# Kernel tuning notes

Measured on AMD Instinct MI355X. Metric: run time of the kernel, lower is better.

The kernel has to match this reference:

```python
import jax, jax.numpy as jnp
import numpy as np

N = 4096; B = 4; NPB = N // B; K = 16
C = 128; COUT = 128; LMAX = 2; L = (LMAX + 1) ** 2  # 9 SH coefficients
H = 8; A = 8; V = 16; HV = H * V
F = 256; NB = 128; FD = 256; CUTOFF = 3.0
E = N * K

def _silu(x):
    return x * jax.nn.sigmoid(x)

def _mish(x):
    return x * jnp.tanh(jax.nn.softplus(x))

def _rms_norm(x, gamma):
    # degree-wise RMS over channel dim, x: [N, L, C]
    s = jnp.sqrt(jnp.mean(x * x, axis=-1, keepdims=True) + 1e-6)
    return x / s * gamma

def _rot_l1(x, R):
    # rotate the l=1 block (coeffs 1:4) of x [E, L, C] by R [E, 3, 3]
    l1 = jnp.einsum('eij,ejc->eic', R, x[:, 1:4, :])
    return jnp.concatenate([x[:, :1, :], l1, x[:, 4:, :]], axis=1)

def _knn(coord, batch):
    d2 = jnp.sum((coord[:, None, :] - coord[None, :, :]) ** 2, axis=-1)  # [N,N]
    same = batch[:, None] == batch[None, :]
    big = jnp.asarray(1e9, d2.dtype)
    d2 = jnp.where(same, d2, big)
    d2 = d2.at[jnp.arange(N), jnp.arange(N)].set(big)
    neg, idx = jax.lax.top_k(-d2, K)
    dist = jnp.sqrt(jnp.maximum(-neg, 0.0))
    edge_src = idx.reshape(-1)                       # [E]
    edge_dst = jnp.repeat(jnp.arange(N), K)          # [E]
    valid = (dist <= CUTOFF).reshape(-1)
    return edge_src, edge_dst, valid

def _edge_rot_mat(edge_vec):
    # deterministic rotation aligning each edge with the y-axis (eSCN-style)
    nx = edge_vec / (jnp.linalg.norm(edge_vec, axis=-1, keepdims=True) + 1e-12)
    ref = jnp.where(jnp.abs(nx[:, :1]) < 0.9,
                    jnp.array([1.0, 0.0, 0.0], nx.dtype),
                    jnp.array([0.0, 1.0, 0.0], nx.dtype))
    nz = jnp.cross(nx, ref)
    nz = nz / (jnp.linalg.norm(nz, axis=-1, keepdims=True) + 1e-12)
    ny = jnp.cross(nz, nx)
    return jnp.stack([nz, nx, ny], axis=1)  # [E,3,3]; R @ edge_dir = e_y

def _forward(node_coord, node_emb, batch, condition,
             W_e1, b_e1, W_e2, b_e2, W_src, W_dst, w_a, W_v, W_o,
             gamma1, gamma2, W_g, W_f1, W_f2, W_film, b_film):
    # dynamic KNN graph; geometry detached as in original (edge_vec.detach())
    coord_g = jax.lax.stop_gradient(node_coord)
    edge_src, edge_dst, valid = _knn(coord_g, batch)
    edge_vec = coord_g[edge_src] - coord_g[edge_dst]                  # [E,3]
    edge_len = jnp.linalg.norm(edge_vec, axis=-1)                     # [E]
    R = _edge_rot_mat(edge_vec)                                       # [E,3,3]
    # gaussian radial basis -> per-edge embedding
    mu = jnp.linspace(0.0, CUTOFF, NB)
    sigma = CUTOFF / NB
    rbf = jnp.exp(-0.5 * ((edge_len[:, None] - mu) / sigma) ** 2)     # [E,NB]
    edge_h = _silu(rbf @ W_e1 + b_e1) @ W_e2 + b_e2                   # [E,HV]
    # equivariant attention (rotate into edge frame, attend, rotate back)
    x_src = _rot_l1(node_emb[edge_src], R)                            # [E,L,C]
    q = node_emb[edge_dst, 0] @ W_dst + x_src[:, 0] @ W_src           # [E,H*A]
    logits = jnp.einsum('eha,ha->eh', _silu(q).reshape(E, H, A), w_a)
    logits = jnp.where(valid[:, None], logits, -1e9)
    m = jax.ops.segment_max(logits, edge_dst, num_segments=N)
    ex = jnp.exp(logits - m[edge_dst])
    den = jax.ops.segment_sum(ex, edge_dst, num_segments=N)
    attn = ex / (den[edge_dst] + 1e-9)                                # [E,H]
    v = jnp.einsum('elc,cv->elv', x_src, W_v) * edge_h[:, None, :]    # [E,L,HV]
    v = v.reshape(E, L, H, V) * attn[:, None, :, None]
    msg = _rot_l1(v.reshape(E, L, HV), jnp.swapaxes(R, 1, 2))         # back to global frame
    agg = jax.ops.segment_sum(msg, edge_dst, num_segments=N)          # [N,L,HV]
    x = node_emb + jnp.einsum('nlv,vc->nlc', agg, W_o)
    # FFN with separable S2 (scalar-gated) activation
    h = _rms_norm(x, gamma2)
    gate = _silu(h[:, 0] @ W_g)                                       # [N,F]
    hid = jnp.einsum('nlc,cf->nlf', h, W_f1) * gate[:, None, :]
    x = x + jnp.einsum('nlf,fo->nlo', hid, W_f2)
    x = _rms_norm(x, gamma1)
    # FiLM conditioning over flattened (L*C) per batch element
    film = _mish(condition) @ W_film + b_film                         # [B, 2*L*COUT]
    w, bfi = film[:, :L * COUT], film[:, L * COUT:]
    c = x.reshape(B, NPB, L * COUT) * w[:, None, :] + bfi[:, None, :]
    return c.reshape(N, L, COUT)

def setup_inputs():
    key = jax.random.key(0)
    ks = jax.random.split(key, 16)
    node_coord = jax.random.uniform(ks[0], (N, 3)) * 2.0
    node_emb = jax.random.normal(ks[1], (N, L, C)) * 0.1
    batch = jnp.arange(N, dtype=jnp.int64 if jax.config.jax_enable_x64 else jnp.int32) // NPB
    condition = jax.random.normal(ks[2], (B, FD))
    s = lambda d: 1.0 / np.sqrt(d)
    return {
        'node_coord': node_coord, 'node_emb': node_emb, 'batch': batch, 'condition': condition,
        'W_e1': jax.random.normal(ks[3], (NB, 128)) * s(NB), 'b_e1': jnp.zeros((128,)),
        'W_e2': jax.random.normal(ks[4], (128, HV)) * s(128), 'b_e2': jnp.zeros((HV,)),
        'W_src': jax.random.normal(ks[5], (C, H * A)) * s(C),
        'W_dst': jax.random.normal(ks[6], (C, H * A)) * s(C),
        'w_a': jax.random.normal(ks[7], (H, A)) * s(A),
        'W_v': jax.random.normal(ks[8], (C, HV)) * s(C),
        'W_o': jax.random.normal(ks[9], (HV, C)) * s(HV),
        'gamma1': jnp.ones((C,)), 'gamma2': jnp.ones((C,)),
        'W_g': jax.random.normal(ks[10], (C, F)) * s(C),
        'W_f1': jax.random.normal(ks[11], (C, F)) * s(C),
        'W_f2': jax.random.normal(ks[12], (F, COUT)) * s(F),
        'W_film': jax.random.normal(ks[13], (FD, 2 * L * COUT)) * s(FD),
        'b_film': jnp.zeros((2 * L * COUT,)),
    }

def reference(node_coord, node_emb, batch, condition,
              W_e1, b_e1, W_e2, b_e2, W_src, W_dst, w_a, W_v, W_o,
              gamma1, gamma2, W_g, W_f1, W_f2, W_film, b_film):
    out = _forward(node_coord, node_emb, batch, condition,
                   W_e1, b_e1, W_e2, b_e2, W_src, W_dst, w_a, W_v, W_o,
                   gamma1, gamma2, W_g, W_f1, W_f2, W_film, b_film)
    return (node_coord, out, batch)
```

## Files before the change

### kernel.cpp

```cpp
#include <hip/hip_runtime.h>

#define NNODE 4096
#define NPB   1024

typedef float v2f __attribute__((ext_vector_type(2)));
typedef float v4f __attribute__((ext_vector_type(4)));

__device__ __forceinline__ float siluf(float x){ return x / (1.0f + expf(-x)); }

__device__ __forceinline__ v2f pk_fma_lo(v2f a, v2f b, v2f c){
  v2f d;
  asm("v_pk_fma_f32 %0, %1, %2, %3 op_sel_hi:[1,0,1]" : "=v"(d) : "v"(a), "v"(b), "v"(c));
  return d;
}
__device__ __forceinline__ v2f pk_fma_hi(v2f a, v2f b, v2f c){
  v2f d;
  asm("v_pk_fma_f32 %0, %1, %2, %3 op_sel:[0,1,0] op_sel_hi:[1,1,1]" : "=v"(d) : "v"(a), "v"(b), "v"(c));
  return d;
}
__device__ __forceinline__ v2f pk_fma2(v2f a, v2f b, v2f c){
  v2f d;
  asm("v_pk_fma_f32 %0, %1, %2, %3" : "=v"(d) : "v"(a), "v"(b), "v"(c));
  return d;
}
#define SHLO(h) __builtin_shufflevector((h), (h), 0, 1)
#define SHHI(h) __builtin_shufflevector((h), (h), 2, 3)

__global__ __launch_bounds__(256) void k_film(const float* __restrict__ cond,
                                              const float* __restrict__ Wfilm,
                                              const float* __restrict__ bfilm,
                                              float* __restrict__ filmG){
  __shared__ float mL[256];
  int b = blockIdx.y;
  int t = threadIdx.x;
  int j = blockIdx.x*256 + t;
  float x = cond[b*256 + t];
  float sp = fmaxf(x, 0.f) + log1pf(expf(-fabsf(x)));
  mL[t] = x * tanhf(sp);
  __syncthreads();
  if(j >= 2304) return;
  float acc = bfilm[j];
  for(int i=0;i<256;i++) acc += mL[i] * Wfilm[i*2304 + j];
  filmG[b*2304 + j] = acc;
}

__global__ __launch_bounds__(256) void k_pre(const float* __restrict__ emb,
                                             const float* __restrict__ Wv,
                                             const float* __restrict__ Wsrc,
                                             const float* __restrict__ Wdst,
                                             float* __restrict__ ZG,
                                             float* __restrict__ QsG,
                                             float* __restrict__ QdG){
  __shared__ __align__(16) float S[4*1152];
  const int t = threadIdx.x;
  const int rg = __builtin_amdgcn_readfirstlane(t >> 6);
  const int lane = t & 63;
  const int c0 = lane*2;
  const int n0 = blockIdx.x*4;
  const int n = n0 + rg;

  {
    const float4* src = (const float4*)(emb + (size_t)n0*1152);
    float4* dst = (float4*)S;
    for(int i=t; i<1152; i+=256) dst[i] = src[i];
  }
  __syncthreads();
  const float* en = &S[rg*1152];

  v2f z[9];
  #pragma unroll
  for(int l=0;l<9;l++) z[l] = (v2f)0.0f;
  for(int c4=0;c4<32;c4++){
    v2f wv0 = *(const v2f*)&Wv[(c4*4+0)*128 + c0];
    v2f wv1 = *(const v2f*)&Wv[(c4*4+1)*128 + c0];
    v2f wv2 = *(const v2f*)&Wv[(c4*4+2)*128 + c0];
    v2f wv3 = *(const v2f*)&Wv[(c4*4+3)*128 + c0];
    #pragma unroll
    for(int l=0;l<9;l++){
      v4f x4 = *(const v4f*)&en[l*128 + c4*4];
      v2f h01 = SHLO(x4), h23 = SHHI(x4);
      z[l] = pk_fma_lo(wv0, h01, z[l]);
      z[l] = pk_fma_hi(wv1, h01, z[l]);
      z[l] = pk_fma_lo(wv2, h23, z[l]);
      z[l] = pk_fma_hi(wv3, h23, z[l]);
    }
  }
  #pragma unroll
  for(int l=0;l<9;l++) *(v2f*)&ZG[(size_t)n*1152 + l*128 + c0] = z[l];

  float qs = 0.f, qd = 0.f;
  for(int c4=0;c4<32;c4++){
    v4f e4 = *(const v4f*)&en[c4*4];
    qs = fmaf(e4.x, Wsrc[(c4*4+0)*64 + lane], qs);
    qs = fmaf(e4.y, Wsrc[(c4*4+1)*64 + lane], qs);
    qs = fmaf(e4.z, Wsrc[(c4*4+2)*64 + lane], qs);
    qs = fmaf(e4.w, Wsrc[(c4*4+3)*64 + lane], qs);
    qd = fmaf(e4.x, Wdst[(c4*4+0)*64 + lane], qd);
    qd = fmaf(e4.y, Wdst[(c4*4+1)*64 + lane], qd);
    qd = fmaf(e4.z, Wdst[(c4*4+2)*64 + lane], qd);
    qd = fmaf(e4.w, Wdst[(c4*4+3)*64 + lane], qd);
  }
  QsG[n*64 + lane] = qs;
  QdG[n*64 + lane] = qd;
}

#define E2_HD   0
#define E2_RB   2048
#define E2_AT   2304
#define E2_KI   2432
#define E2_LEN  2448
#define E2_VL   2464
#define E2_W0   2480
#define F_ACT   0
#define F_HID   1152
#define E2_NPF  2560
__global__ __launch_bounds__(128, 4) void k_node(
    const float* __restrict__ coord,
    const float* __restrict__ emb,
    const float* __restrict__ We1, const float* __restrict__ be1,
    const float* __restrict__ We2, const float* __restrict__ be2,
    const float* __restrict__ wa,
    const float* __restrict__ Wo,
    const float* __restrict__ g1, const float* __restrict__ g2,
    const float* __restrict__ Wg, const float* __restrict__ Wf1,
    const float* __restrict__ Wf2,
    const float* __restrict__ Qs, const float* __restrict__ Qd,
    const float* __restrict__ Z,
    const float* __restrict__ filmG,
    float* __restrict__ out){
  __shared__ __align__(16) float S[2*E2_NPF];
  int* Si = (int*)S;
  const int t = threadIdx.x;
  const int w = __builtin_amdgcn_readfirstlane(t >> 6);
  const int lane = t & 63;
  const int bid = blockIdx.x;
  const int sbid = (bid & 7) * (NNODE/16) + (bid >> 3);
  const int n = sbid*2 + w;
  const int base = n & ~(NPB - 1);
  const int self = n - base;
  const int NP = w * E2_NPF;
  const int c0 = lane*2;
  const int myh = lane >> 3;

  {
    const float* cb = coord + (size_t)base*3;
    const float cx = cb[self*3+0];
    const float cy = cb[self*3+1];
    const float cz = cb[self*3+2];
    float d2a[16]; int ida[16];
    #pragma unroll
    for(int q=0;q<16;q++){
      int j = lane + q*64;
      float dx = __fsub_rn(cb[j*3+0], cx);
      float dy = __fsub_rn(cb[j*3+1], cy);
      float dz = __fsub_rn(cb[j*3+2], cz);
      float d2 = __fadd_rn(__fadd_rn(__fmul_rn(dx,dx), __fmul_rn(dy,dy)), __fmul_rn(dz,dz));
      if(j == self) d2 = 3e38f;
      d2a[q] = d2; ida[q] = j;
    }
    #pragma unroll 1
    for(int r=0;r<16;r++){
      float bd = d2a[0]; int bi = ida[0];
      #pragma unroll
      for(int q=1;q<16;q++){
        bool bet = (d2a[q] < bd) || (d2a[q] == bd && ida[q] < bi);
        if(bet){ bd = d2a[q]; bi = ida[q]; }
      }
      #pragma unroll
      for(int s=1;s<64;s<<=1){
        float od = __shfl_xor(bd, s, 64);
        int   oi = __shfl_xor(bi, s, 64);
        bool bet = (od < bd) || (od == bd && oi < bi);
        if(bet){ bd = od; bi = oi; }
      }
      if(lane == 0){
        Si[NP + E2_KI + r] = bi;
        float len = __fsqrt_rn(bd);
        S[NP + E2_LEN + r] = len;
        S[NP + E2_VL + r]  = (len <= 3.0f) ? 1.0f : 0.0f;
        int i0 = (int)(len * (127.0f/3.0f) + 0.5f);
        int w0 = i0 - 7;
        w0 = w0 < 0 ? 0 : (w0 > 112 ? 112 : w0);
        Si[NP + E2_W0 + r] = w0;
      }
      #pragma unroll
      for(int q=0;q<16;q++) if(ida[q] == bi) d2a[q] = 3e38f;
    }
  }
  __syncthreads();

  {
    const int e0 = lane >> 3, hh = lane & 7;
    float4 qda = *(const float4*)&Qd[(size_t)n*64 + hh*8];
    float4 qdb = *(const float4*)&Qd[(size_t)n*64 + hh*8 + 4];
    float4 waa = *(const float4*)&wa[hh*8];
    float4 wab = *(const float4*)&wa[hh*8 + 4];
    float lg[2];
    #pragma unroll
    for(int s=0;s<2;s++){
      int e = e0 + s*8;
      int src = base + Si[NP + E2_KI + e];
      float4 qa = *(const float4*)&Qs[(size_t)src*64 + hh*8];
      float4 qb = *(const float4*)&Qs[(size_t)src*64 + hh*8 + 4];
      float sv = siluf(qda.x+qa.x)*waa.x + siluf(qda.y+qa.y)*waa.y
               + siluf(qda.z+qa.z)*waa.z + siluf(qda.w+qa.w)*waa.w
               + siluf(qdb.x+qb.x)*wab.x + siluf(qdb.y+qb.y)*wab.y
               + siluf(qdb.z+qb.z)*wab.z + siluf(qdb.w+qb.w)*wab.w;
      lg[s] = (S[NP + E2_VL + e] > 0.5f) ? sv : -1e9f;
    }
    float m = fmaxf(lg[0], lg[1]);
    m = fmaxf(m, __shfl_xor(m, 8, 64));
    m = fmaxf(m, __shfl_xor(m, 16, 64));
    m = fmaxf(m, __shfl_xor(m, 32, 64));
    float ex0 = expf(lg[0] - m), ex1 = expf(lg[1] - m);
    float den = ex0 + ex1;
    den += __shfl_xor(den, 8, 64);
    den += __shfl_xor(den, 16, 64);
    den += __shfl_xor(den, 32, 64);
    float inv = 1.0f/(den + 1e-9f);
    S[NP + E2_AT + lane]      = ex0*inv;
    S[NP + E2_AT + 64 + lane] = ex1*inv;

    const float step = 3.0f/127.0f;
    const float sigma = 3.0f/128.0f;
    #pragma unroll
    for(int k=0;k<4;k++){
      int idx = lane + k*64;
      int e = idx >> 4, wi = idx & 15;
      float len = S[NP + E2_LEN + e];
      int bin = Si[NP + E2_W0 + e] + wi;
      float d = (len - step*(float)bin) / sigma;
      S[NP + E2_RB + idx] = expf(-0.5f*d*d);
    }
  }
  __syncthreads();

  {
    float a4[16][2]; int b0e[16];
    #pragma unroll
    for(int e=0;e<16;e++){ a4[e][0]=0.f; a4[e][1]=0.f; b0e[e] = Si[NP + E2_W0 + e]; }
    #pragma unroll 1
    for(int wi=0; wi<16; wi++){
      #pragma unroll
      for(int e=0;e<16;e++){
        float rb = S[NP + E2_RB + e*16 + wi];
        float2 we = *(const float2*)&We1[(size_t)(b0e[e] + wi)*128 + c0];
        a4[e][0] = fmaf(rb, we.x, a4[e][0]);
        a4[e][1] = fmaf(rb, we.y, a4[e][1]);
      }
    }
    float2 b1v = *(const float2*)&be1[c0];
    #pragma unroll
    for(int e=0;e<16;e++){
      float2 o; o.x = siluf(a4[e][0] + b1v.x); o.y = siluf(a4[e][1] + b1v.y);
      *(float2*)&S[NP + E2_HD + e*128 + c0] = o;
    }
  }
  __syncthreads();

  v2f a5[16];
  #pragma unroll
  for(int e=0;e<16;e++) a5[e] = (v2f)0.0f;
  #pragma unroll 1
  for(int c4=0;c4<32;c4++){
    v2f w0 = *(const v2f*)&We2[(c4*4+0)*128 + c0];
    v2f w1 = *(const v2f*)&We2[(c4*4+1)*128 + c0];
    v2f w2 = *(const v2f*)&We2[(c4*4+2)*128 + c0];
    v2f w3 = *(const v2f*)&We2[(c4*4+3)*128 + c0];
    #pragma unroll
    for(int e=0;e<16;e++){
      v4f h4 = *(const v4f*)&S[NP + E2_HD + e*128 + c4*4];
      v2f h01 = SHLO(h4), h23 = SHHI(h4);
      a5[e] = pk_fma_lo(w0, h01, a5[e]);
      a5[e] = pk_fma_hi(w1, h01, a5[e]);
      a5[e] = pk_fma_lo(w2, h23, a5[e]);
      a5[e] = pk_fma_hi(w3, h23, a5[e]);
    }
  }

  {
    v2f b2v = *(const v2f*)&be2[c0];
    v2f ag[9];
    #pragma unroll
    for(int l=0;l<9;l++) ag[l] = (v2f)0.0f;
    #pragma unroll 4
    for(int e=0;e<16;e++){
      int src = base + Si[NP + E2_KI + e];
      const float* zp = &Z[(size_t)src*1152 + c0];
      float at = S[NP + E2_AT + e*8 + myh];
      v2f sc = (a5[e] + b2v) * at;
      #pragma unroll
      for(int l=0;l<9;l++){
        v2f z2 = *(const v2f*)&zp[l*128];
        ag[l] = pk_fma2(z2, sc, ag[l]);
      }
    }
    #pragma unroll
    for(int l=0;l<9;l++) *(v2f*)&S[NP + F_ACT + l*128 + c0] = ag[l];
  }

  float* W_ = &S[NP];

  v2f x[9];
  #pragma unroll
  for(int l=0;l<9;l++) x[l] = (v2f)0.0f;
  #pragma unroll 1
  for(int c4=0;c4<32;c4++){
    v2f w0 = *(const v2f*)&Wo[(c4*4+0)*128 + c0];
    v2f w1 = *(const v2f*)&Wo[(c4*4+1)*128 + c0];
    v2f w2 = *(const v2f*)&Wo[(c4*4+2)*128 + c0];
    v2f w3 = *(const v2f*)&Wo[(c4*4+3)*128 + c0];
    #pragma unroll
    for(int l=0;l<9;l++){
      v4f a4 = *(const v4f*)&W_[F_ACT + l*128 + c4*4];
      v2f h01 = SHLO(a4), h23 = SHHI(a4);
      x[l] = pk_fma_lo(w0, h01, x[l]);
      x[l] = pk_fma_hi(w1, h01, x[l]);
      x[l] = pk_fma_lo(w2, h23, x[l]);
      x[l] = pk_fma_hi(w3, h23, x[l]);
    }
  }

  {
    float g2a = g2[c0], g2b = g2[c0+1];
    #pragma unroll
    for(int l=0;l<9;l++){
      v2f e2 = *(const v2f*)&emb[(size_t)n*1152 + l*128 + c0];
      x[l] += e2;
      float sq = x[l][0]*x[l][0] + x[l][1]*x[l][1];
      #pragma unroll
      for(int s=1;s<64;s<<=1) sq += __shfl_xor(sq, s, 64);
      float ss = sqrtf(sq/128.f + 1e-6f);
      v2f o; o.x = x[l][0]/ss*g2a; o.y = x[l][1]/ss*g2b;
      *(v2f*)&W_[F_ACT + l*128 + c0] = o;
    }
  }

  #pragma unroll 1
  for(int ft=0;ft<2;ft++){
    v2f ha[9]; v2f ga = (v2f)0.0f;
    #pragma unroll
    for(int l=0;l<9;l++) ha[l] = (v2f)0.0f;
    #pragma unroll 1
    for(int c4=0;c4<32;c4++){
      v2f wf0 = *(const v2f*)&Wf1[(c4*4+0)*256 + ft*128 + c0];
      v2f wf1 = *(const v2f*)&Wf1[(c4*4+1)*256 + ft*128 + c0];
      v2f wf2 = *(const v2f*)&Wf1[(c4*4+2)*256 + ft*128 + c0];
      v2f wf3 = *(const v2f*)&Wf1[(c4*4+3)*256 + ft*128 + c0];
      v2f wg0 = *(const v2f*)&Wg [(c4*4+0)*256 + ft*128 + c0];
      v2f wg1 = *(const v2f*)&Wg [(c4*4+1)*256 + ft*128 + c0];
      v2f wg2 = *(const v2f*)&Wg [(c4*4+2)*256 + ft*128 + c0];
      v2f wg3 = *(const v2f*)&Wg [(c4*4+3)*256 + ft*128 + c0];
      v4f h0 = *(const v4f*)&W_[F_ACT + 0*128 + c4*4];
      v2f h01 = SHLO(h0), h23 = SHHI(h0);
      ga = pk_fma_lo(wg0, h01, ga);
      ga = pk_fma_hi(wg1, h01, ga);
      ga = pk_fma_lo(wg2, h23, ga);
      ga = pk_fma_hi(wg3, h23, ga);
      ha[0] = pk_fma_lo(wf0, h01, ha[0]);
      ha[0] = pk_fma_hi(wf1, h01, ha[0]);
      ha[0] = pk_fma_lo(wf2, h23, ha[0]);
      ha[0] = pk_fma_hi(wf3, h23, ha[0]);
      #pragma unroll
      for(int l=1;l<9;l++){
        v4f h4 = *(const v4f*)&W_[F_ACT + l*128 + c4*4];
        v2f a01 = SHLO(h4), a23 = SHHI(h4);
        ha[l] = pk_fma_lo(wf0, a01, ha[l]);
        ha[l] = pk_fma_hi(wf1, a01, ha[l]);
        ha[l] = pk_fma_lo(wf2, a23, ha[l]);
        ha[l] = pk_fma_hi(wf3, a23, ha[l]);
      }
    }
    float gx = siluf(ga[0]), gy = siluf(ga[1]);
    #pragma unroll
    for(int l=0;l<9;l++){
      v2f o; o.x = ha[l][0]*gx; o.y = ha[l][1]*gy;
      *(v2f*)&W_[F_HID + l*128 + c0] = o;
    }
    #pragma unroll 1
    for(int f4=0;f4<32;f4++){
      v2f w0 = *(const v2f*)&Wf2[(ft*128 + f4*4+0)*128 + c0];
      v2f w1 = *(const v2f*)&Wf2[(ft*128 + f4*4+1)*128 + c0];
      v2f w2 = *(const v2f*)&Wf2[(ft*128 + f4*4+2)*128 + c0];
      v2f w3 = *(const v2f*)&Wf2[(ft*128 + f4*4+3)*128 + c0];
      #pragma unroll
      for(int l=0;l<9;l++){
        v4f h4 = *(const v4f*)&W_[F_HID + l*128 + f4*4];
        v2f h01 = SHLO(h4), h23 = SHHI(h4);
        x[l] = pk_fma_lo(w0, h01, x[l]);
        x[l] = pk_fma_hi(w1, h01, x[l]);
        x[l] = pk_fma_lo(w2, h23, x[l]);
        x[l] = pk_fma_hi(w3, h23, x[l]);
      }
    }
  }

  {
    float g1a = g1[c0], g1b = g1[c0+1];
    int b = n >> 10;
    #pragma unroll
    for(int l=0;l<9;l++){
      float sq = x[l][0]*x[l][0] + x[l][1]*x[l][1];
      #pragma unroll
      for(int s=1;s<64;s<<=1) sq += __shfl_xor(sq, s, 64);
      float ss = sqrtf(sq/128.f + 1e-6f);
      v2f fw = *(const v2f*)&filmG[b*2304 + l*128 + c0];
      v2f fb = *(const v2f*)&filmG[b*2304 + 1152 + l*128 + c0];
      v2f o;
      o.x = x[l][0]/ss*g1a*fw.x + fb.x;
      o.y = x[l][1]/ss*g1b*fw.y + fb.y;
      *(v2f*)&out[12288 + (size_t)n*1152 + l*128 + c0] = o;
    }
  }
}

__global__ __launch_bounds__(256) void k_copy(const float* __restrict__ coord,
                                              float* __restrict__ out){
  int i = blockIdx.x*256 + threadIdx.x;
  if(i < 12288) out[i] = coord[i];
  int n = i - 12288;
  if(n >= 0 && n < 4096) out[12288 + 4718592 + n] = (float)(n >> 10);
}

extern "C" void kernel_launch(void* const* d_in, const int* in_sizes, int n_in,
                              void* d_out, int out_size, void* d_ws, size_t ws_size,
                              hipStream_t stream) {
  const float* coord = (const float*)d_in[0];
  const float* emb   = (const float*)d_in[1];
  const float* cond  = (const float*)d_in[3];
  const float* We1   = (const float*)d_in[4];
  const float* be1   = (const float*)d_in[5];
  const float* We2   = (const float*)d_in[6];
  const float* be2   = (const float*)d_in[7];
  const float* Wsrc  = (const float*)d_in[8];
  const float* Wdst  = (const float*)d_in[9];
  const float* wa    = (const float*)d_in[10];
  const float* Wv    = (const float*)d_in[11];
  const float* Wo    = (const float*)d_in[12];
  const float* g1    = (const float*)d_in[13];
  const float* g2    = (const float*)d_in[14];
  const float* Wg    = (const float*)d_in[15];
  const float* Wf1   = (const float*)d_in[16];
  const float* Wf2   = (const float*)d_in[17];
  const float* Wfilm = (const float*)d_in[18];
  const float* bfilm = (const float*)d_in[19];

  float* outf  = (float*)d_out;
  float* filmG = (float*)d_ws;
  float* QsG   = filmG + 9216;
  float* QdG   = QsG + 262144;
  float* ZG    = QdG + 262144;

  k_film<<<dim3(9,4), 256, 0, stream>>>(cond, Wfilm, bfilm, filmG);
  k_pre<<<NNODE/4, 256, 0, stream>>>(emb, Wv, Wsrc, Wdst, ZG, QsG, QdG);
  k_node<<<NNODE/2, 128, 0, stream>>>(coord, emb,
                                      We1, be1, We2, be2, wa,
                                      Wo, g1, g2, Wg, Wf1, Wf2,
                                      QsG, QdG, ZG, filmG, outf);
  k_copy<<<64, 256, 0, stream>>>(coord, outf);
}
```

Measured before the change: 361.3 us.

## Broadcast node activations via readlane into SGPRs instead of LDS round-trips

Replaces the LDS staging of per-node activations (aggregated messages, normalized hidden, gated FFN hidden) with v_readlane broadcasts into scalar registers that feed packed FMAs directly. This removes LDS stores, LDS vector loads and the implied barriers in the three dense matmul chains. The cost is many readlane instructions (four per FMA group) on the scalar path, possible VALU-to-SGPR hazard stalls, and heavier register pressure from holding activations in VGPRs. Correctness depends on each wavefront holding a whole node's 128 channels, two per lane.

```diff
diff --git a/kernel.cpp b/kernel.cpp
--- a/kernel.cpp
+++ b/kernel.cpp
@@ -22,6 +22,14 @@
   v2f d;
   asm("v_pk_fma_f32 %0, %1, %2, %3" : "=v"(d) : "v"(a), "v"(b), "v"(c));
   return d;
+}
+__device__ __forceinline__ v2f pk_fma_sb(v2f a, unsigned long long b, v2f c){
+  v2f d;
+  asm("v_pk_fma_f32 %0, %1, %2, %3 op_sel_hi:[1,0,1]" : "=v"(d) : "v"(a), "s"(b), "v"(c));
+  return d;
+}
+__device__ __forceinline__ unsigned long long rlz(float v, int ln){
+  return (unsigned long long)(unsigned int)__builtin_amdgcn_readlane(__float_as_int(v), ln);
 }
 #define SHLO(h) __builtin_shufflevector((h), (h), 0, 1)
 #define SHHI(h) __builtin_shufflevector((h), (h), 2, 3)
@@ -111,8 +119,6 @@
 #define E2_LEN  2448
 #define E2_VL   2464
 #define E2_W0   2480
-#define F_ACT   0
-#define F_HID   1152
 #define E2_NPF  2560
 __global__ __launch_bounds__(128, 4) void k_node(
     const float* __restrict__ coord,
@@ -278,9 +284,9 @@
     }
   }
 
+  v2f ag[9];
   {
     v2f b2v = *(const v2f*)&be2[c0];
-    v2f ag[9];
     #pragma unroll
     for(int l=0;l<9;l++) ag[l] = (v2f)0.0f;
     #pragma unroll 4
@@ -295,32 +301,33 @@
         ag[l] = pk_fma2(z2, sc, ag[l]);
       }
     }
-    #pragma unroll
-    for(int l=0;l<9;l++) *(v2f*)&S[NP + F_ACT + l*128 + c0] = ag[l];
-  }
-
-  float* W_ = &S[NP];
+  }
+
 
   v2f x[9];
   #pragma unroll
   for(int l=0;l<9;l++) x[l] = (v2f)0.0f;
   #pragma unroll 1
   for(int c4=0;c4<32;c4++){
+    int ln0 = c4*2, ln1 = ln0+1;
     v2f w0 = *(const v2f*)&Wo[(c4*4+0)*128 + c0];
     v2f w1 = *(const v2f*)&Wo[(c4*4+1)*128 + c0];
     v2f w2 = *(const v2f*)&Wo[(c4*4+2)*128 + c0];
     v2f w3 = *(const v2f*)&Wo[(c4*4+3)*128 + c0];
     #pragma unroll
     for(int l=0;l<9;l++){
-      v4f a4 = *(const v4f*)&W_[F_ACT + l*128 + c4*4];
-      v2f h01 = SHLO(a4), h23 = SHHI(a4);
-      x[l] = pk_fma_lo(w0, h01, x[l]);
-      x[l] = pk_fma_hi(w1, h01, x[l]);
-      x[l] = pk_fma_lo(w2, h23, x[l]);
-      x[l] = pk_fma_hi(w3, h23, x[l]);
-    }
-  }
-
+      unsigned long long h0 = rlz(ag[l][0], ln0);
+      unsigned long long h1 = rlz(ag[l][1], ln0);
+      unsigned long long h2 = rlz(ag[l][0], ln1);
+      unsigned long long h3 = rlz(ag[l][1], ln1);
+      x[l] = pk_fma_sb(w0, h0, x[l]);
+      x[l] = pk_fma_sb(w1, h1, x[l]);
+      x[l] = pk_fma_sb(w2, h2, x[l]);
+      x[l] = pk_fma_sb(w3, h3, x[l]);
+    }
+  }
+
+  v2f hl[9];
   {
     float g2a = g2[c0], g2b = g2[c0+1];
     #pragma unroll
@@ -331,8 +338,8 @@
       #pragma unroll
       for(int s=1;s<64;s<<=1) sq += __shfl_xor(sq, s, 64);
       float ss = sqrtf(sq/128.f + 1e-6f);
-      v2f o; o.x = x[l][0]/ss*g2a; o.y = x[l][1]/ss*g2b;
-      *(v2f*)&W_[F_ACT + l*128 + c0] = o;
+      hl[l][0] = x[l][0]/ss*g2a;
+      hl[l][1] = x[l][1]/ss*g2b;
     }
   }
 
@@ -343,6 +350,7 @@
     for(int l=0;l<9;l++) ha[l] = (v2f)0.0f;
     #pragma unroll 1
     for(int c4=0;c4<32;c4++){
+      int ln0 = c4*2, ln1 = ln0+1;
       v2f wf0 = *(const v2f*)&Wf1[(c4*4+0)*256 + ft*128 + c0];
       v2f wf1 = *(const v2f*)&Wf1[(c4*4+1)*256 + ft*128 + c0];
       v2f wf2 = *(const v2f*)&Wf1[(c4*4+2)*256 + ft*128 + c0];
@@ -351,46 +359,52 @@
       v2f wg1 = *(const v2f*)&Wg [(c4*4+1)*256 + ft*128 + c0];
       v2f wg2 = *(const v2f*)&Wg [(c4*4+2)*256 + ft*128 + c0];
       v2f wg3 = *(const v2f*)&Wg [(c4*4+3)*256 + ft*128 + c0];
-      v4f h0 = *(const v4f*)&W_[F_ACT + 0*128 + c4*4];
-      v2f h01 = SHLO(h0), h23 = SHHI(h0);
-      ga = pk_fma_lo(wg0, h01, ga);
-      ga = pk_fma_hi(wg1, h01, ga);
-      ga = pk_fma_lo(wg2, h23, ga);
-      ga = pk_fma_hi(wg3, h23, ga);
-      ha[0] = pk_fma_lo(wf0, h01, ha[0]);
-      ha[0] = pk_fma_hi(wf1, h01, ha[0]);
-      ha[0] = pk_fma_lo(wf2, h23, ha[0]);
-      ha[0] = pk_fma_hi(wf3, h23, ha[0]);
+      {
+        unsigned long long h0 = rlz(hl[0][0], ln0);
+        unsigned long long h1 = rlz(hl[0][1], ln0);
+        unsigned long long h2 = rlz(hl[0][0], ln1);
+        unsigned long long h3 = rlz(hl[0][1], ln1);
+        ga = pk_fma_sb(wg0, h0, ga);
+        ga = pk_fma_sb(wg1, h1, ga);
+        ga = pk_fma_sb(wg2, h2, ga);
+        ga = pk_fma_sb(wg3, h3, ga);
+        ha[0] = pk_fma_sb(wf0, h0, ha[0]);
+        ha[0] = pk_fma_sb(wf1, h1, ha[0]);
+        ha[0] = pk_fma_sb(wf2, h2, ha[0]);
+        ha[0] = pk_fma_sb(wf3, h3, ha[0]);
+      }
       #pragma unroll
       for(int l=1;l<9;l++){
-        v4f h4 = *(const v4f*)&W_[F_ACT + l*128 + c4*4];
-        v2f a01 = SHLO(h4), a23 = SHHI(h4);
-        ha[l] = pk_fma_lo(wf0, a01, ha[l]);
-        ha[l] = pk_fma_hi(wf1, a01, ha[l]);
-        ha[l] = pk_fma_lo(wf2, a23, ha[l]);
-        ha[l] = pk_fma_hi(wf3, a23, ha[l]);
+        unsigned long long h0 = rlz(hl[l][0], ln0);
+        unsigned long long h1 = rlz(hl[l][1], ln0);
+        unsigned long long h2 = rlz(hl[l][0], ln1);
+        unsigned long long h3 = rlz(hl[l][1], ln1);
+        ha[l] = pk_fma_sb(wf0, h0, ha[l]);
+        ha[l] = pk_fma_sb(wf1, h1, ha[l]);
+        ha[l] = pk_fma_sb(wf2, h2, ha[l]);
+        ha[l] = pk_fma_sb(wf3, h3, ha[l]);
       }
     }
     float gx = siluf(ga[0]), gy = siluf(ga[1]);
     #pragma unroll
-    for(int l=0;l<9;l++){
-      v2f o; o.x = ha[l][0]*gx; o.y = ha[l][1]*gy;
-      *(v2f*)&W_[F_HID + l*128 + c0] = o;
-    }
+    for(int l=0;l<9;l++){ ha[l][0] *= gx; ha[l][1] *= gy; }
     #pragma unroll 1
     for(int f4=0;f4<32;f4++){
+      int ln0 = f4*2, ln1 = ln0+1;
       v2f w0 = *(const v2f*)&Wf2[(ft*128 + f4*4+0)*128 + c0];
       v2f w1 = *(const v2f*)&Wf2[(ft*128 + f4*4+1)*128 + c0];
       v2f w2 = *(const v2f*)&Wf2[(ft*128 + f4*4+2)*128 + c0];
       v2f w3 = *(const v2f*)&Wf2[(ft*128 + f4*4+3)*128 + c0];
       #pragma unroll
       for(int l=0;l<9;l++){
-        v4f h4 = *(const v4f*)&W_[F_HID + l*128 + f4*4];
-        v2f h01 = SHLO(h4), h23 = SHHI(h4);
-        x[l] = pk_fma_lo(w0, h01, x[l]);
-        x[l] = pk_fma_hi(w1, h01, x[l]);
-        x[l] = pk_fma_lo(w2, h23, x[l]);
-        x[l] = pk_fma_hi(w3, h23, x[l]);
+        unsigned long long h0 = rlz(ha[l][0], ln0);
+        unsigned long long h1 = rlz(ha[l][1], ln0);
+        unsigned long long h2 = rlz(ha[l][0], ln1);
+        unsigned long long h3 = rlz(ha[l][1], ln1);
+        x[l] = pk_fma_sb(w0, h0, x[l]);
+        x[l] = pk_fma_sb(w1, h1, x[l]);
+        x[l] = pk_fma_sb(w2, h2, x[l]);
+        x[l] = pk_fma_sb(w3, h3, x[l]);
       }
     }
   }
```

Measured after the change: 406.3 us. 1.12x slower.

## Fuse FiLM and copy kernels into neighbors; merge FFN first-layer halves

Applied to the files above, without the earlier changes.

The FiLM projection becomes extra blocks of the pre-projection kernel, and the coord/batch copy moves into the tail of the node kernel, cutting launches from four to two. The FFN first layer now computes both 128-wide halves of the hidden dimension in a single pass over the normalized activations, so they are read from shared memory once instead of twice. This doubles the live accumulators (ha0/ha1), which raises register pressure and may lower occupancy or cause spills.

```diff
diff --git a/kernel.cpp b/kernel.cpp
--- a/kernel.cpp
+++ b/kernel.cpp
@@ -26,37 +26,41 @@
 #define SHLO(h) __builtin_shufflevector((h), (h), 0, 1)
 #define SHHI(h) __builtin_shufflevector((h), (h), 2, 3)
 
-__global__ __launch_bounds__(256) void k_film(const float* __restrict__ cond,
-                                              const float* __restrict__ Wfilm,
-                                              const float* __restrict__ bfilm,
-                                              float* __restrict__ filmG){
-  __shared__ float mL[256];
-  int b = blockIdx.y;
-  int t = threadIdx.x;
-  int j = blockIdx.x*256 + t;
-  float x = cond[b*256 + t];
-  float sp = fmaxf(x, 0.f) + log1pf(expf(-fabsf(x)));
-  mL[t] = x * tanhf(sp);
-  __syncthreads();
-  if(j >= 2304) return;
-  float acc = bfilm[j];
-  for(int i=0;i<256;i++) acc += mL[i] * Wfilm[i*2304 + j];
-  filmG[b*2304 + j] = acc;
-}
-
 __global__ __launch_bounds__(256) void k_pre(const float* __restrict__ emb,
                                              const float* __restrict__ Wv,
                                              const float* __restrict__ Wsrc,
                                              const float* __restrict__ Wdst,
+                                             const float* __restrict__ cond,
+                                             const float* __restrict__ Wfilm,
+                                             const float* __restrict__ bfilm,
                                              float* __restrict__ ZG,
                                              float* __restrict__ QsG,
-                                             float* __restrict__ QdG){
+                                             float* __restrict__ QdG,
+                                             float* __restrict__ filmG){
   __shared__ __align__(16) float S[4*1152];
   const int t = threadIdx.x;
+  const int bidx = blockIdx.x;
+
+  if(bidx >= 1024){
+    int fb = bidx - 1024;
+    int b  = fb / 9;
+    int jb = fb % 9;
+    int j  = jb*256 + t;
+    float x = cond[b*256 + t];
+    float sp = fmaxf(x, 0.f) + log1pf(expf(-fabsf(x)));
+    S[t] = x * tanhf(sp);
+    __syncthreads();
+    if(j >= 2304) return;
+    float acc = bfilm[j];
+    for(int i=0;i<256;i++) acc += S[i] * Wfilm[i*2304 + j];
+    filmG[b*2304 + j] = acc;
+    return;
+  }
+
   const int rg = __builtin_amdgcn_readfirstlane(t >> 6);
   const int lane = t & 63;
   const int c0 = lane*2;
-  const int n0 = blockIdx.x*4;
+  const int n0 = bidx*4;
   const int n = n0 + rg;
 
   {
@@ -336,45 +340,68 @@
     }
   }
 
+  v2f ha0[9], ha1[9]; v2f ga0 = (v2f)0.0f, ga1 = (v2f)0.0f;
+  #pragma unroll
+  for(int l=0;l<9;l++){ ha0[l] = (v2f)0.0f; ha1[l] = (v2f)0.0f; }
+  #pragma unroll 1
+  for(int c4=0;c4<32;c4++){
+    v2f wfa0 = *(const v2f*)&Wf1[(c4*4+0)*256 + c0];
+    v2f wfa1 = *(const v2f*)&Wf1[(c4*4+1)*256 + c0];
+    v2f wfa2 = *(const v2f*)&Wf1[(c4*4+2)*256 + c0];
+    v2f wfa3 = *(const v2f*)&Wf1[(c4*4+3)*256 + c0];
+    v2f wfb0 = *(const v2f*)&Wf1[(c4*4+0)*256 + 128 + c0];
+    v2f wfb1 = *(const v2f*)&Wf1[(c4*4+1)*256 + 128 + c0];
+    v2f wfb2 = *(const v2f*)&Wf1[(c4*4+2)*256 + 128 + c0];
+    v2f wfb3 = *(const v2f*)&Wf1[(c4*4+3)*256 + 128 + c0];
+    v2f wga0 = *(const v2f*)&Wg[(c4*4+0)*256 + c0];
+    v2f wga1 = *(const v2f*)&Wg[(c4*4+1)*256 + c0];
+    v2f wga2 = *(const v2f*)&Wg[(c4*4+2)*256 + c0];
+    v2f wga3 = *(const v2f*)&Wg[(c4*4+3)*256 + c0];
+    v2f wgb0 = *(const v2f*)&Wg[(c4*4+0)*256 + 128 + c0];
+    v2f wgb1 = *(const v2f*)&Wg[(c4*4+1)*256 + 128 + c0];
+    v2f wgb2 = *(const v2f*)&Wg[(c4*4+2)*256 + 128 + c0];
+    v2f wgb3 = *(const v2f*)&Wg[(c4*4+3)*256 + 128 + c0];
+    v4f h0 = *(const v4f*)&W_[F_ACT + 0*128 + c4*4];
+    v2f h01 = SHLO(h0), h23 = SHHI(h0);
+    ga0 = pk_fma_lo(wga0, h01, ga0);
+    ga0 = pk_fma_hi(wga1, h01, ga0);
+    ga0 = pk_fma_lo(wga2, h23, ga0);
+    ga0 = pk_fma_hi(wga3, h23, ga0);
+    ga1 = pk_fma_lo(wgb0, h01, ga1);
+    ga1 = pk_fma_hi(wgb1, h01, ga1);
+    ga1 = pk_fma_lo(wgb2, h23, ga1);
+    ga1 = pk_fma_hi(wgb3, h23, ga1);
+    ha0[0] = pk_fma_lo(wfa0, h01, ha0[0]);
+    ha0[0] = pk_fma_hi(wfa1, h01, ha0[0]);
+    ha0[0] = pk_fma_lo(wfa2, h23, ha0[0]);
+    ha0[0] = pk_fma_hi(wfa3, h23, ha0[0]);
+    ha1[0] = pk_fma_lo(wfb0, h01, ha1[0]);
+    ha1[0] = pk_fma_hi(wfb1, h01, ha1[0]);
+    ha1[0] = pk_fma_lo(wfb2, h23, ha1[0]);
+    ha1[0] = pk_fma_hi(wfb3, h23, ha1[0]);
+    #pragma unroll
+    for(int l=1;l<9;l++){
+      v4f h4 = *(const v4f*)&W_[F_ACT + l*128 + c4*4];
+      v2f a01 = SHLO(h4), a23 = SHHI(h4);
+      ha0[l] = pk_fma_lo(wfa0, a01, ha0[l]);
+      ha0[l] = pk_fma_hi(wfa1, a01, ha0[l]);
+      ha0[l] = pk_fma_lo(wfa2, a23, ha0[l]);
+      ha0[l] = pk_fma_hi(wfa3, a23, ha0[l]);
+      ha1[l] = pk_fma_lo(wfb0, a01, ha1[l]);
+      ha1[l] = pk_fma_hi(wfb1, a01, ha1[l]);
+      ha1[l] = pk_fma_lo(wfb2, a23, ha1[l]);
+      ha1[l] = pk_fma_hi(wfb3, a23, ha1[l]);
+    }
+  }
+
   #pragma unroll 1
   for(int ft=0;ft<2;ft++){
-    v2f ha[9]; v2f ga = (v2f)0.0f;
-    #pragma unroll
-    for(int l=0;l<9;l++) ha[l] = (v2f)0.0f;
-    #pragma unroll 1
-    for(int c4=0;c4<32;c4++){
-      v2f wf0 = *(const v2f*)&Wf1[(c4*4+0)*256 + ft*128 + c0];
-      v2f wf1 = *(const v2f*)&Wf1[(c4*4+1)*256 + ft*128 + c0];
-      v2f wf2 = *(const v2f*)&Wf1[(c4*4+2)*256 + ft*128 + c0];
-      v2f wf3 = *(const v2f*)&Wf1[(c4*4+3)*256 + ft*128 + c0];
-      v2f wg0 = *(const v2f*)&Wg [(c4*4+0)*256 + ft*128 + c0];
-      v2f wg1 = *(const v2f*)&Wg [(c4*4+1)*256 + ft*128 + c0];
-      v2f wg2 = *(const v2f*)&Wg [(c4*4+2)*256 + ft*128 + c0];
-      v2f wg3 = *(const v2f*)&Wg [(c4*4+3)*256 + ft*128 + c0];
-      v4f h0 = *(const v4f*)&W_[F_ACT + 0*128 + c4*4];
-      v2f h01 = SHLO(h0), h23 = SHHI(h0);
-      ga = pk_fma_lo(wg0, h01, ga);
-      ga = pk_fma_hi(wg1, h01, ga);
-      ga = pk_fma_lo(wg2, h23, ga);
-      ga = pk_fma_hi(wg3, h23, ga);
-      ha[0] = pk_fma_lo(wf0, h01, ha[0]);
-      ha[0] = pk_fma_hi(wf1, h01, ha[0]);
-      ha[0] = pk_fma_lo(wf2, h23, ha[0]);
-      ha[0] = pk_fma_hi(wf3, h23, ha[0]);
-      #pragma unroll
-      for(int l=1;l<9;l++){
-        v4f h4 = *(const v4f*)&W_[F_ACT + l*128 + c4*4];
-        v2f a01 = SHLO(h4), a23 = SHHI(h4);
-        ha[l] = pk_fma_lo(wf0, a01, ha[l]);
-        ha[l] = pk_fma_hi(wf1, a01, ha[l]);
-        ha[l] = pk_fma_lo(wf2, a23, ha[l]);
-        ha[l] = pk_fma_hi(wf3, a23, ha[l]);
-      }
-    }
+    v2f ga = ft ? ga1 : ga0;
     float gx = siluf(ga[0]), gy = siluf(ga[1]);
     #pragma unroll
     for(int l=0;l<9;l++){
-      v2f o; o.x = ha[l][0]*gx; o.y = ha[l][1]*gy;
+      v2f hv = ft ? ha1[l] : ha0[l];
+      v2f o; o.x = hv[0]*gx; o.y = hv[1]*gy;
       *(v2f*)&W_[F_HID + l*128 + c0] = o;
     }
     #pragma unroll 1
@@ -412,14 +439,9 @@
       *(v2f*)&out[12288 + (size_t)n*1152 + l*128 + c0] = o;
     }
   }
-}
-
-__global__ __launch_bounds__(256) void k_copy(const float* __restrict__ coord,
-                                              float* __restrict__ out){
-  int i = blockIdx.x*256 + threadIdx.x;
-  if(i < 12288) out[i] = coord[i];
-  int n = i - 12288;
-  if(n >= 0 && n < 4096) out[12288 + 4718592 + n] = (float)(n >> 10);
+
+  if(lane < 3) out[(size_t)n*3 + lane] = coord[(size_t)n*3 + lane];
+  if(lane == 3) out[12288 + 4718592 + n] = (float)(n >> 10);
 }
 
 extern "C" void kernel_launch(void* const* d_in, const int* in_sizes, int n_in,
@@ -451,11 +473,11 @@
   float* QdG   = QsG + 262144;
   float* ZG    = QdG + 262144;
 
-  k_film<<<dim3(9,4), 256, 0, stream>>>(cond, Wfilm, bfilm, filmG);
-  k_pre<<<NNODE/4, 256, 0, stream>>>(emb, Wv, Wsrc, Wdst, ZG, QsG, QdG);
+  k_pre<<<1024 + 36, 256, 0, stream>>>(emb, Wv, Wsrc, Wdst,
+                                       cond, Wfilm, bfilm,
+                                       ZG, QsG, QdG, filmG);
   k_node<<<NNODE/2, 128, 0, stream>>>(coord, emb,
                                       We1, be1, We2, be2, wa,
                                       Wo, g1, g2, Wg, Wf1, Wf2,
                                       QsG, QdG, ZG, filmG, outf);
-  k_copy<<<64, 256, 0, stream>>>(coord, outf);
-}
+}
```

Measured after the change: 384.7 us. +6.5%, slower.
